# Performance work log

Measured on AMD Instinct MI355X. Metric: run time of the kernel, lower is better.

## Reference

```python
import math
import jax, jax.numpy as jnp
import numpy as np

B, C, K, P, STRIDE, ITERS = 32, 32, 3, 4, 2, 3
PSIZE = P * P
EPS = 1e-6
LAMBDA = 1e-3
LN_2PI = math.log(2.0 * math.pi)


def _extract_patches(x, K, stride):
    # Replicates torch F.unfold + transpose + view exactly, including the
    # layout reinterpretation: unfold's channel dim is ordered (c, kh, kw)
    # (c slowest) but the torch code views it as (K*K, c).
    b, h, w, c = x.shape
    pad = K // 2
    oh = (h + 2 * pad - K) // stride + 1
    ow = (w + 2 * pad - K) // stride + 1
    xp = jnp.pad(x, ((0, 0), (pad, pad), (pad, pad), (0, 0)))
    sl = []
    for kh in range(K):
        for kw in range(K):
            sl.append(xp[:, kh:kh + stride * (oh - 1) + 1:stride,
                            kw:kw + stride * (ow - 1) + 1:stride, :])
    p = jnp.stack(sl, axis=-1)                 # (b, oh, ow, c, K*K)  -> (c, kh, kw) order
    p = p.reshape(b, oh, ow, c * K * K)        # flat, c slowest (matches torch unfold memory)
    patches = p.reshape(b, oh, ow, K * K, c)   # reinterpret as (K*K, c), as the torch view does
    return patches, oh, ow


def _em_routing(v, a_in, beta_u, beta_a):
    # v: (b, Bin, C, psize), a_in: (b, Bin, 1)
    b, Bin, Cc, psize = v.shape
    r = jnp.full((b, Bin, Cc, 1), 1.0 / Cc, dtype=v.dtype)
    a4 = a_in[:, :, None, :]                   # (b, Bin, 1, 1)
    a_out = None
    mu = None
    for t in range(ITERS):
        # ---- M step ----
        rr = r * a4
        rr = rr / (jnp.sum(rr, axis=2, keepdims=True) + EPS)
        r_sum = jnp.sum(rr, axis=1, keepdims=True)            # (b,1,C,1)
        coeff = rr / (r_sum + EPS)
        mu = jnp.sum(coeff * v, axis=1, keepdims=True)        # (b,1,C,psize)
        sigma_sq = jnp.sum(coeff * (v - mu) ** 2, axis=1, keepdims=True) + EPS
        sigma_sq = jnp.maximum(sigma_sq, 1e-4)
        r_sum_flat = r_sum.reshape(b, Cc, 1)
        sig_flat = jnp.maximum(sigma_sq.reshape(b, Cc, psize), 1e-4)
        cost_h = (beta_u.reshape(1, Cc, 1) + jnp.log(jnp.sqrt(sig_flat))) * r_sum_flat
        a_out = jax.nn.sigmoid(LAMBDA * (beta_a.reshape(1, Cc) - jnp.sum(cost_h, axis=2)))
        a_out = jnp.clip(a_out, 1e-4, 1.0 - 1e-4)
        mu = jnp.nan_to_num(mu, nan=0.0, posinf=1e4, neginf=-1e4)
        sigma_sq = jnp.nan_to_num(sigma_sq, nan=1e-4, posinf=1e4, neginf=1e-4)
        a_out = jnp.nan_to_num(a_out, nan=0.5, posinf=1.0 - 1e-4, neginf=1e-4)
        # ---- E step ----
        if t < ITERS - 1:
            ss = jnp.maximum(sigma_sq, 1e-4)
            ao = jnp.clip(a_out, 1e-4, 1.0 - 1e-4)
            ln_p = -(v - mu) ** 2 / (2.0 * ss) - jnp.log(jnp.sqrt(ss)) - 0.5 * LN_2PI
            ln_ap = jnp.sum(ln_p, axis=3) + jnp.log(ao.reshape(b, 1, Cc) + EPS)
            ln_ap = jnp.nan_to_num(ln_ap, nan=0.0, posinf=50.0, neginf=-50.0)
            r = jax.nn.softmax(ln_ap, axis=2)[..., None]
            r = jnp.nan_to_num(r, nan=1.0 / Cc, posinf=1.0, neginf=0.0)
    p_out = jnp.nan_to_num(mu[:, 0], nan=0.0, posinf=1e4, neginf=-1e4)  # (b, C, psize)
    a_out = jnp.nan_to_num(a_out, nan=0.5, posinf=1.0 - 1e-4, neginf=1e-4)
    return p_out, a_out


def setup_inputs() -> dict:
    key = jax.random.key(0)
    k1, k2 = jax.random.split(key)
    x = jax.random.normal(k1, (2, 16, 16, B * (PSIZE + 1)), dtype=jnp.float32)
    weights = jax.random.normal(k2, (1, K * K * B, C, PSIZE, PSIZE), dtype=jnp.float32) * 0.02
    beta_u = jnp.zeros((C,), dtype=jnp.float32)
    beta_a = jnp.zeros((C,), dtype=jnp.float32)
    return {"x": x, "weights": weights, "beta_u": beta_u, "beta_a": beta_a}


def reference(x, weights, beta_u, beta_a):
    b, h, w, c = x.shape
    patches, oh, ow = _extract_patches(x, K, STRIDE)          # (b,oh,ow,K*K,c)
    p_in = patches[..., :B * PSIZE].reshape(b * oh * ow, K * K * B, PSIZE)
    a_in = patches[..., B * PSIZE:].reshape(b * oh * ow, K * K * B, 1)
    w0 = weights[0]                                           # (K*K*B, C, psize, psize)
    v = jnp.einsum('bip,icpq->bicq', p_in, w0)                # (b*, K*K*B, C, psize)
    p_out, a_out = _em_routing(v, a_in, beta_u, beta_a)
    p_out = p_out.reshape(b, oh, ow, C * PSIZE)
    a_out = a_out.reshape(b, oh, ow, C)
    out = jnp.concatenate([p_out, a_out], axis=3)
    return p_out, a_out, out
```

## Files before the change

kernel.cpp:

```cpp
#include <hip/hip_runtime.h>
#include <hip/hip_bf16.h>
#include <math.h>

#define EPSV 1e-6f
#define LAMBDAV 1e-3f
#define LN_2PI 1.8378770664093453f

__device__ __forceinline__ float bflo(unsigned int u) {
    union { unsigned int i; float f; } x; x.i = u << 16; return x.f;
}
__device__ __forceinline__ float bfhi(unsigned int u) {
    union { unsigned int i; float f; } x; x.i = u & 0xffff0000u; return x.f;
}
__device__ __forceinline__ unsigned short f2bf(float f) {
    __hip_bfloat16 h = __float2bfloat16(f);
    return *(unsigned short*)&h;
}

typedef __attribute__((ext_vector_type(8))) short s8v;
typedef __attribute__((ext_vector_type(4))) float f4v;
typedef __attribute__((ext_vector_type(2))) int i2v;

template<int CTRL>
__device__ __forceinline__ float dpp_mv(float x) {
    return __int_as_float(__builtin_amdgcn_update_dpp(
        0, __float_as_int(x), CTRL, 0xF, 0xF, true));
}
__device__ __forceinline__ float x16_sum(float x) {
#if __has_builtin(__builtin_amdgcn_permlane16_swap)
    i2v r = __builtin_amdgcn_permlane16_swap(__float_as_int(x), __float_as_int(x), false, false);
    return __int_as_float(r.x) + __int_as_float(r.y);
#else
    return x + __int_as_float(__builtin_amdgcn_ds_swizzle(__float_as_int(x), 0x401F));
#endif
}
__device__ __forceinline__ float x16_max(float x) {
#if __has_builtin(__builtin_amdgcn_permlane16_swap)
    i2v r = __builtin_amdgcn_permlane16_swap(__float_as_int(x), __float_as_int(x), false, false);
    return fmaxf(__int_as_float(r.x), __int_as_float(r.y));
#else
    return fmaxf(x, __int_as_float(__builtin_amdgcn_ds_swizzle(__float_as_int(x), 0x401F)));
#endif
}
__device__ __forceinline__ float xhalf_sum(float x) {
#if __has_builtin(__builtin_amdgcn_permlane32_swap)
    i2v r = __builtin_amdgcn_permlane32_swap(__float_as_int(x), __float_as_int(x), false, false);
    return __int_as_float(r.x) + __int_as_float(r.y);
#else
    return x + __shfl_xor(x, 32, 64);
#endif
}
__device__ __forceinline__ float red_max32(float x) {
    x = fmaxf(x, dpp_mv<0xB1>(x));
    x = fmaxf(x, dpp_mv<0x4E>(x));
    x = fmaxf(x, dpp_mv<0x124>(x));
    x = fmaxf(x, dpp_mv<0x128>(x));
    return x16_max(x);
}
__device__ __forceinline__ float red_sum32(float x) {
    x += dpp_mv<0xB1>(x);
    x += dpp_mv<0x4E>(x);
    x += dpp_mv<0x124>(x);
    x += dpp_mv<0x128>(x);
    return x16_sum(x);
}
__device__ __forceinline__ float red_sum16(float x) {
    x += dpp_mv<0xB1>(x);
    x += dpp_mv<0x4E>(x);
    x += dpp_mv<0x124>(x);
    x += dpp_mv<0x128>(x);
    return x;
}

__global__ __launch_bounds__(256)
void conv_v_kernel(const float* __restrict__ x, const float* __restrict__ w,
                   __hip_bfloat16* __restrict__ vout)
{
    __shared__ unsigned short wb[512 * 40];
    __shared__ unsigned short pb[128 * 40];

    const int i2  = blockIdx.x;
    const int tid = threadIdx.x;

    for (int u = tid; u < 512 * 8; u += 256) {
        int r = u >> 3, j = u & 7;
        *(unsigned int*)&wb[r * 40 + 16 + j * 2] = 0;
    }
    for (int u = tid; u < 128 * 8; u += 256) {
        int r = u >> 3, j = u & 7;
        *(unsigned int*)&pb[r * 40 + 16 + j * 2] = 0;
    }
    #pragma unroll 4
    for (int u = 0; u < 32; ++u) {
        int idx = u * 256 + tid;
        int c = idx >> 8, p = (idx >> 4) & 15, q = idx & 15;
        wb[(c * 16 + q) * 40 + p] = f2bf(w[(size_t)i2 * 8192 + idx]);
    }
    #pragma unroll
    for (int u = 0; u < 8; ++u) {
        int idx = u * 256 + tid;
        int nn = idx >> 4, p = idx & 15;
        int e  = i2 * 16 + p;
        int k2 = e >> 9, c2 = e & 511;
        int f  = k2 * 544 + c2;
        int ci = f / 9, kk = f - ci * 9;
        int bi = nn >> 6, oi = (nn >> 3) & 7, oj = nn & 7;
        int row = 2 * oi + kk / 3 - 1;
        int col = 2 * oj + (kk - (kk / 3) * 3) - 1;
        float val = 0.f;
        if ((unsigned)row < 16u && (unsigned)col < 16u)
            val = x[((bi * 16 + row) * 16 + col) * 544 + ci];
        pb[nn * 40 + p] = f2bf(val);
    }
    __syncthreads();

    const int lane = tid & 63;
    const int wv   = tid >> 6;
    const int l16  = lane & 15;
    const int quad = lane >> 4;
    const int cq0  = wv * 128;

    s8v afrag[8], bfrag[8];
    #pragma unroll
    for (int mt = 0; mt < 8; ++mt)
        afrag[mt] = *(const s8v*)&wb[(cq0 + mt * 16 + l16) * 40 + quad * 8];
    #pragma unroll
    for (int nt = 0; nt < 8; ++nt)
        bfrag[nt] = *(const s8v*)&pb[(nt * 16 + l16) * 40 + quad * 8];

    #pragma unroll
    for (int nt = 0; nt < 8; ++nt) {
        const int nl = nt * 16 + l16;
        #pragma unroll
        for (int mt = 0; mt < 8; ++mt) {
            f4v acc = {0.f, 0.f, 0.f, 0.f};
            acc = __builtin_amdgcn_mfma_f32_16x16x32_bf16(afrag[mt], bfrag[nt], acc, 0, 0, 0);
            int cq = cq0 + mt * 16 + quad * 4;
            unsigned int lo = f2bf(acc[0]) | ((unsigned int)f2bf(acc[1]) << 16);
            unsigned int hi = f2bf(acc[2]) | ((unsigned int)f2bf(acc[3]) << 16);
            uint2 pk; pk.x = lo; pk.y = hi;
            *(uint2*)((unsigned short*)vout + ((size_t)nl * 288 + i2) * 512 + cq) = pk;
        }
    }
}

__global__ __launch_bounds__(1024, 4)
void em_routing_kernel(const float* __restrict__ x,
                       const unsigned short* __restrict__ v,
                       const float* __restrict__ beta_u,
                       const float* __restrict__ beta_a,
                       float* __restrict__ out)
{
    __shared__ float fct_s[288];
    __shared__ float red_s[16 * 64 * 17];
    __shared__ float mu_s[32 * 17];
    __shared__ float i2ss_s[32 * 17];
    __shared__ float aout_s[32];
    __shared__ float kc_s[32];

    const int n   = blockIdx.x;
    const int tid = threadIdx.x;
    const int bi = n >> 6, oi = (n >> 3) & 7, oj = n & 7;

    if (tid < 288) {
        int k2 = tid >> 5;
        int c2 = 512 + (tid & 31);
        int f  = k2 * 544 + c2;
        int ci = f / 9;
        int kk = f - ci * 9;
        int row = 2 * oi + kk / 3 - 1;
        int col = 2 * oj + (kk - (kk / 3) * 3) - 1;
        float a = 0.f;
        if ((unsigned)row < 16u && (unsigned)col < 16u)
            a = x[((bi * 16 + row) * 16 + col) * 544 + ci];
        fct_s[tid] = a / (a + EPSV);
    }
    __syncthreads();

    const unsigned short* vb = v + (size_t)n * 288 * 512;
    const int wv   = tid >> 6;
    const int lane = tid & 63;
    const int c    = lane & 31;
    const int qh   = lane >> 5;
    const int qb   = qh * 8;
    const unsigned short* base = vb + c * 16 + qb;

    for (int t = 0; t < 3; ++t) {
        float mu8[8], is8[8], kcv = 0.f;
        if (t > 0) {
            #pragma unroll
            for (int j = 0; j < 8; ++j) {
                mu8[j] = mu_s[c * 17 + qb + j];
                is8[j] = i2ss_s[c * 17 + qb + j];
            }
            kcv = kc_s[c];
        }

        float s0 = 0.f, s1[8], s2[8];
        #pragma unroll
        for (int j = 0; j < 8; ++j) { s1[j] = 0.f; s2[j] = 0.f; }

        uint4 ua = *(const uint4*)(base + (size_t)(0 * 16 + wv) * 512);
        uint4 ub = *(const uint4*)(base + (size_t)(1 * 16 + wv) * 512);

        for (int kp = 0; kp < 9; ++kp) {
            const int ia = (2 * kp) * 16 + wv;
            const int ib = (2 * kp + 1) * 16 + wv;
            uint4 una, unb;
            if (kp < 8) {
                una = *(const uint4*)(base + (size_t)((2 * kp + 2) * 16 + wv) * 512);
                unb = *(const uint4*)(base + (size_t)((2 * kp + 3) * 16 + wv) * 512);
            }
            float va[8], vvb[8];
            va[0] = bflo(ua.x); va[1] = bfhi(ua.x);
            va[2] = bflo(ua.y); va[3] = bfhi(ua.y);
            va[4] = bflo(ua.z); va[5] = bfhi(ua.z);
            va[6] = bflo(ua.w); va[7] = bfhi(ua.w);
            vvb[0] = bflo(ub.x); vvb[1] = bfhi(ub.x);
            vvb[2] = bflo(ub.y); vvb[3] = bfhi(ub.y);
            vvb[4] = bflo(ub.z); vvb[5] = bfhi(ub.z);
            vvb[6] = bflo(ub.w); vvb[7] = bfhi(ub.w);

            float rra, rrb;
            if (t == 0) {
                rra = fct_s[ia] * 0.03125f;
                rrb = fct_s[ib] * 0.03125f;
            } else {
                float pa = 0.f, pb2 = 0.f;
                #pragma unroll
                for (int j = 0; j < 8; ++j) {
                    float da = va[j] - mu8[j];
                    float db = vvb[j] - mu8[j];
                    pa  += da * da * is8[j];
                    pb2 += db * db * is8[j];
                }
                pa  = xhalf_sum(pa);
                pb2 = xhalf_sum(pb2);
                float acca = kcv - pa;
                float accb = kcv - pb2;
                float mxa = red_max32(acca);
                float mxb = red_max32(accb);
                float ea = __expf(acca - mxa);
                float eb = __expf(accb - mxb);
                float sa = red_sum32(ea);
                float sb = red_sum32(eb);
                rra = (ea / sa) * fct_s[ia];
                rrb = (eb / sb) * fct_s[ib];
            }

            s0 += rra + rrb;
            #pragma unroll
            for (int j = 0; j < 8; ++j) {
                s1[j] += rra * va[j] + rrb * vvb[j];
                s2[j] += rra * va[j] * va[j] + rrb * vvb[j] * vvb[j];
            }
            ua = una; ub = unb;
        }

        {
            float* dst = &red_s[(wv * 64 + lane) * 17];
            dst[0] = s0;
            #pragma unroll
            for (int j = 0; j < 8; ++j) { dst[1 + j] = s1[j]; dst[9 + j] = s2[j]; }
        }
        __syncthreads();

        if (tid < 512) {
            const int c2 = tid >> 4, q2 = tid & 15;
            const int qh2 = q2 >> 3, j2 = q2 & 7;
            float S0 = 0.f, S1 = 0.f, S2 = 0.f;
            #pragma unroll
            for (int wvi = 0; wvi < 16; ++wvi) {
                S0 += red_s[(wvi * 64 + c2) * 17];
                const float* sp = &red_s[(wvi * 64 + qh2 * 32 + c2) * 17];
                S1 += sp[1 + j2];
                S2 += sp[9 + j2];
            }
            float invr = 1.0f / (S0 + EPSV);
            float w0  = S0 * invr;
            float m   = S1 * invr;
            float s2p = S2 * invr;
            float sig = s2p - m * m * (2.0f - w0);
            sig = fmaxf(sig + EPSV, 1e-4f);
            float hl = 0.5f * logf(sig);
            mu_s[c2 * 17 + q2]   = m;
            i2ss_s[c2 * 17 + q2] = 1.0f / (2.0f * sig);
            float shl = red_sum16(hl);
            if (q2 == 0) {
                float bu  = beta_u[c2];
                float cs  = (16.0f * bu + shl) * S0;
                float arg = LAMBDAV * (beta_a[c2] - cs);
                float ao  = 1.0f / (1.0f + expf(-arg));
                ao = fminf(fmaxf(ao, 1e-4f), 1.0f - 1e-4f);
                aout_s[c2] = ao;
                kc_s[c2]   = logf(ao + EPSV) - shl - 8.0f * LN_2PI;
            }
        }
        __syncthreads();
    }

    if (tid < 512) {
        int c2 = tid >> 4, q2 = tid & 15;
        float mu = mu_s[c2 * 17 + q2];
        if (isnan(mu)) mu = 0.f;
        mu = fminf(fmaxf(mu, -10000.f), 10000.f);
        out[(size_t)n * 512 + tid] = mu;
        out[69632 + (size_t)n * 544 + tid] = mu;
        if (tid < 32) {
            float ao = aout_s[tid];
            if (isnan(ao)) ao = 0.5f;
            out[65536 + n * 32 + tid] = ao;
            out[69632 + n * 544 + 512 + tid] = ao;
        }
    }
}

extern "C" void kernel_launch(void* const* d_in, const int* in_sizes, int n_in,
                              void* d_out, int out_size, void* d_ws, size_t ws_size,
                              hipStream_t stream) {
    const float* x  = (const float*)d_in[0];
    const float* w  = (const float*)d_in[1];
    const float* bu = (const float*)d_in[2];
    const float* ba = (const float*)d_in[3];
    float* out = (float*)d_out;
    __hip_bfloat16* v = (__hip_bfloat16*)d_ws;

    conv_v_kernel<<<dim3(288), dim3(256), 0, stream>>>(x, w, v);
    em_routing_kernel<<<dim3(128), dim3(1024), 0, stream>>>(
        x, (const unsigned short*)v, bu, ba, out);
}
```

Baseline: 126.3 us.

## Split EM routing across block pairs with global partial-sum exchange

The conv kernel now splits each input capsule's output channels across two blocks, doubling its grid. The EM routing kernel splits the 18 input-capsule groups of each output position across two blocks. Each block publishes partial sums to a global workspace and waits on a spin flag for its peer before finishing every iteration. This raises occupancy across the GPU's CUs, at the cost of a global round-trip and spin-wait sync per iteration. It also relies on both blocks of a pair being co-resident, and adds LDS padding to limit blocks per CU.

Measured after the change: 166.9 us. 1.32x slower.

```diff
diff --git a/kernel.cpp b/kernel.cpp
--- a/kernel.cpp
+++ b/kernel.cpp
@@ -72,17 +72,30 @@
     return x;
 }
 
+__device__ __forceinline__ void g_store(float* p, float v) {
+    __hip_atomic_store(p, v, __ATOMIC_RELAXED, __HIP_MEMORY_SCOPE_AGENT);
+}
+__device__ __forceinline__ float g_load(const float* p) {
+    return __hip_atomic_load(p, __ATOMIC_RELAXED, __HIP_MEMORY_SCOPE_AGENT);
+}
+
 __global__ __launch_bounds__(256)
 void conv_v_kernel(const float* __restrict__ x, const float* __restrict__ w,
-                   __hip_bfloat16* __restrict__ vout)
+                   __hip_bfloat16* __restrict__ vout, unsigned int* __restrict__ flags)
 {
-    __shared__ unsigned short wb[512 * 40];
+    __shared__ unsigned short wb[256 * 40];
     __shared__ unsigned short pb[128 * 40];
 
-    const int i2  = blockIdx.x;
+    const int bid = blockIdx.x;
+    const int i2  = bid >> 1;
+    const int mh  = bid & 1;
     const int tid = threadIdx.x;
 
-    for (int u = tid; u < 512 * 8; u += 256) {
+    if (bid == 0) {
+        for (int u = tid; u < 384; u += 256) flags[u] = 0;
+    }
+
+    for (int u = tid; u < 256 * 8; u += 256) {
         int r = u >> 3, j = u & 7;
         *(unsigned int*)&wb[r * 40 + 16 + j * 2] = 0;
     }
@@ -91,10 +104,10 @@
         *(unsigned int*)&pb[r * 40 + 16 + j * 2] = 0;
     }
     #pragma unroll 4
-    for (int u = 0; u < 32; ++u) {
+    for (int u = 0; u < 16; ++u) {
         int idx = u * 256 + tid;
-        int c = idx >> 8, p = (idx >> 4) & 15, q = idx & 15;
-        wb[(c * 16 + q) * 40 + p] = f2bf(w[(size_t)i2 * 8192 + idx]);
+        int cl = idx >> 8, p = (idx >> 4) & 15, q = idx & 15;
+        wb[(cl * 16 + q) * 40 + p] = f2bf(w[(size_t)i2 * 8192 + mh * 4096 + idx]);
     }
     #pragma unroll
     for (int u = 0; u < 8; ++u) {
@@ -118,12 +131,12 @@
     const int wv   = tid >> 6;
     const int l16  = lane & 15;
     const int quad = lane >> 4;
-    const int cq0  = wv * 128;
-
-    s8v afrag[8], bfrag[8];
+    const int cq0l = wv * 64;
+
+    s8v afrag[4], bfrag[8];
     #pragma unroll
-    for (int mt = 0; mt < 8; ++mt)
-        afrag[mt] = *(const s8v*)&wb[(cq0 + mt * 16 + l16) * 40 + quad * 8];
+    for (int mt = 0; mt < 4; ++mt)
+        afrag[mt] = *(const s8v*)&wb[(cq0l + mt * 16 + l16) * 40 + quad * 8];
     #pragma unroll
     for (int nt = 0; nt < 8; ++nt)
         bfrag[nt] = *(const s8v*)&pb[(nt * 16 + l16) * 40 + quad * 8];
@@ -132,10 +145,10 @@
     for (int nt = 0; nt < 8; ++nt) {
         const int nl = nt * 16 + l16;
         #pragma unroll
-        for (int mt = 0; mt < 8; ++mt) {
+        for (int mt = 0; mt < 4; ++mt) {
             f4v acc = {0.f, 0.f, 0.f, 0.f};
             acc = __builtin_amdgcn_mfma_f32_16x16x32_bf16(afrag[mt], bfrag[nt], acc, 0, 0, 0);
-            int cq = cq0 + mt * 16 + quad * 4;
+            int cq = mh * 256 + cq0l + mt * 16 + quad * 4;
             unsigned int lo = f2bf(acc[0]) | ((unsigned int)f2bf(acc[1]) << 16);
             unsigned int hi = f2bf(acc[2]) | ((unsigned int)f2bf(acc[3]) << 16);
             uint2 pk; pk.x = lo; pk.y = hi;
@@ -149,6 +162,8 @@
                        const unsigned short* __restrict__ v,
                        const float* __restrict__ beta_u,
                        const float* __restrict__ beta_a,
+                       float* __restrict__ part,
+                       unsigned int* __restrict__ flags,
                        float* __restrict__ out)
 {
     __shared__ float fct_s[288];
@@ -157,10 +172,14 @@
     __shared__ float i2ss_s[32 * 17];
     __shared__ float aout_s[32];
     __shared__ float kc_s[32];
-
-    const int n   = blockIdx.x;
+    __shared__ float pad_s[1600];
+
+    const int bid = blockIdx.x;
+    const int n   = bid & 127;
+    const int h   = bid >> 7;
     const int tid = threadIdx.x;
     const int bi = n >> 6, oi = (n >> 3) & 7, oj = n & 7;
+    if (tid == 1023) pad_s[0] = 0.f;
 
     if (tid < 288) {
         int k2 = tid >> 5;
@@ -183,6 +202,7 @@
     const int c    = lane & 31;
     const int qh   = lane >> 5;
     const int qb   = qh * 8;
+    const int kbase = 9 * h;
     const unsigned short* base = vb + c * 16 + qb;
 
     for (int t = 0; t < 3; ++t) {
@@ -200,16 +220,19 @@
         #pragma unroll
         for (int j = 0; j < 8; ++j) { s1[j] = 0.f; s2[j] = 0.f; }
 
-        uint4 ua = *(const uint4*)(base + (size_t)(0 * 16 + wv) * 512);
-        uint4 ub = *(const uint4*)(base + (size_t)(1 * 16 + wv) * 512);
-
-        for (int kp = 0; kp < 9; ++kp) {
-            const int ia = (2 * kp) * 16 + wv;
-            const int ib = (2 * kp + 1) * 16 + wv;
+        uint4 ua = *(const uint4*)(base + (size_t)((kbase + 0) * 16 + wv) * 512);
+        uint4 ub = *(const uint4*)(base + (size_t)((kbase + 1) * 16 + wv) * 512);
+
+        for (int kp = 0; kp < 4; ++kp) {
+            const int ia = (kbase + 2 * kp) * 16 + wv;
+            const int ib = ia + 16;
             uint4 una, unb;
-            if (kp < 8) {
-                una = *(const uint4*)(base + (size_t)((2 * kp + 2) * 16 + wv) * 512);
-                unb = *(const uint4*)(base + (size_t)((2 * kp + 3) * 16 + wv) * 512);
+            if (kp < 3) {
+                una = *(const uint4*)(base + (size_t)(ia + 32) * 512);
+                unb = *(const uint4*)(base + (size_t)(ia + 48) * 512);
+            } else {
+                una = *(const uint4*)(base + (size_t)((kbase + 8) * 16 + wv) * 512);
+                unb = una;
             }
             float va[8], vvb[8];
             va[0] = bflo(ua.x); va[1] = bfhi(ua.x);
@@ -256,6 +279,37 @@
             }
             ua = una; ub = unb;
         }
+        {
+            const int ia = (kbase + 8) * 16 + wv;
+            float va[8];
+            va[0] = bflo(ua.x); va[1] = bfhi(ua.x);
+            va[2] = bflo(ua.y); va[3] = bfhi(ua.y);
+            va[4] = bflo(ua.z); va[5] = bfhi(ua.z);
+            va[6] = bflo(ua.w); va[7] = bfhi(ua.w);
+            float rra;
+            if (t == 0) {
+                rra = fct_s[ia] * 0.03125f;
+            } else {
+                float pa = 0.f;
+                #pragma unroll
+                for (int j = 0; j < 8; ++j) {
+                    float da = va[j] - mu8[j];
+                    pa += da * da * is8[j];
+                }
+                pa = xhalf_sum(pa);
+                float acca = kcv - pa;
+                float mxa = red_max32(acca);
+                float ea = __expf(acca - mxa);
+                float sa = red_sum32(ea);
+                rra = (ea / sa) * fct_s[ia];
+            }
+            s0 += rra;
+            #pragma unroll
+            for (int j = 0; j < 8; ++j) {
+                s1[j] += rra * va[j];
+                s2[j] += rra * va[j] * va[j];
+            }
+        }
 
         {
             float* dst = &red_s[(wv * 64 + lane) * 17];
@@ -265,10 +319,14 @@
         }
         __syncthreads();
 
+        float* gp_own        = part + (((size_t)t * 128 + n) * 2 + h) * 1088;
+        const float* gp_peer = part + (((size_t)t * 128 + n) * 2 + (1 - h)) * 1088;
+        unsigned int* flg    = flags + t * 128 + n;
+
+        float S0 = 0.f, S1 = 0.f, S2 = 0.f;
         if (tid < 512) {
             const int c2 = tid >> 4, q2 = tid & 15;
             const int qh2 = q2 >> 3, j2 = q2 & 7;
-            float S0 = 0.f, S1 = 0.f, S2 = 0.f;
             #pragma unroll
             for (int wvi = 0; wvi < 16; ++wvi) {
                 S0 += red_s[(wvi * 64 + c2) * 17];
@@ -276,6 +334,24 @@
                 S1 += sp[1 + j2];
                 S2 += sp[9 + j2];
             }
+            g_store(gp_own + tid, S1);
+            g_store(gp_own + 512 + tid, S2);
+            if (q2 == 0) g_store(gp_own + 1024 + c2, S0);
+        }
+        __syncthreads();
+        if (tid == 0) {
+            __hip_atomic_fetch_add(flg, 1u, __ATOMIC_RELEASE, __HIP_MEMORY_SCOPE_AGENT);
+            int guard = 0;
+            while (__hip_atomic_load(flg, __ATOMIC_ACQUIRE, __HIP_MEMORY_SCOPE_AGENT) < 2u
+                   && guard < (1 << 22)) { __builtin_amdgcn_s_sleep(2); ++guard; }
+        }
+        __syncthreads();
+
+        if (tid < 512) {
+            const int c2 = tid >> 4, q2 = tid & 15;
+            S1 += g_load(gp_peer + tid);
+            S2 += g_load(gp_peer + 512 + tid);
+            S0 += g_load(gp_peer + 1024 + c2);
             float invr = 1.0f / (S0 + EPSV);
             float w0  = S0 * invr;
             float m   = S1 * invr;
@@ -299,7 +375,7 @@
         __syncthreads();
     }
 
-    if (tid < 512) {
+    if (h == 0 && tid < 512) {
         int c2 = tid >> 4, q2 = tid & 15;
         float mu = mu_s[c2 * 17 + q2];
         if (isnan(mu)) mu = 0.f;
@@ -324,8 +400,10 @@
     const float* ba = (const float*)d_in[3];
     float* out = (float*)d_out;
     __hip_bfloat16* v = (__hip_bfloat16*)d_ws;
-
-    conv_v_kernel<<<dim3(288), dim3(256), 0, stream>>>(x, w, v);
-    em_routing_kernel<<<dim3(128), dim3(1024), 0, stream>>>(
-        x, (const unsigned short*)v, bu, ba, out);
-}
+    float* part        = (float*)((char*)d_ws + (38u << 20));
+    unsigned int* flags = (unsigned int*)((char*)d_ws + (43u << 20));
+
+    conv_v_kernel<<<dim3(576), dim3(256), 0, stream>>>(x, w, v, flags);
+    em_routing_kernel<<<dim3(256), dim3(1024), 0, stream>>>(
+        x, (const unsigned short*)v, bu, ba, part, flags, out);
+}
```
